# Kernel optimization log

Measured on AMD Instinct MI355X. Metric: run time of the kernel, lower is better.

## Reference

```python
import jax, jax.numpy as jnp
import numpy as np

INDIM = 256
NUM_CENTERS = 1024
OUTDIM = 128
N = 65536


def setup_inputs() -> dict:
    key = jax.random.key(0)
    kx, kc, kw, kb = jax.random.split(key, 4)
    x = jax.random.normal(kx, (N, INDIM), dtype=jnp.float32)
    # centers ~ U(-1, 1), sigmas = 0.1 as in init_centers_sigmas
    centers = jax.random.uniform(kc, (NUM_CENTERS, INDIM), dtype=jnp.float32, minval=-1.0, maxval=1.0)
    sigmas = jnp.full((NUM_CENTERS,), 0.1, dtype=jnp.float32)
    # nn.Linear(num_centers, outdim): weight [outdim, num_centers], bias [outdim]
    bound = 1.0 / np.sqrt(NUM_CENTERS)
    W = jax.random.uniform(kw, (OUTDIM, NUM_CENTERS), dtype=jnp.float32, minval=-bound, maxval=bound)
    b = jax.random.uniform(kb, (OUTDIM,), dtype=jnp.float32, minval=-bound, maxval=bound)
    return {"x": x, "centers": centers, "sigmas": sigmas, "W": W, "b": b}


def reference(x, centers, sigmas, W, b):
    # phi[n, m] = exp(-sigma_m * ||x_n - c_m||^2)
    x_sq = jnp.sum(x * x, axis=1)               # [N]
    c_sq = jnp.sum(centers * centers, axis=1)   # [M]
    cross = jnp.einsum('nd,md->nm', x, centers) # [N, M]
    sqdist = x_sq[:, None] + c_sq[None, :] - 2.0 * cross
    phi = jnp.exp(-sigmas[None, :] * sqdist)    # [N, M]
    return phi @ W.T + b                        # [N, outdim]
```

## Files before the change

kernel.cpp:

```cpp
#include <hip/hip_runtime.h>

typedef __attribute__((ext_vector_type(8))) short bf16x8;
typedef __attribute__((ext_vector_type(4))) float f32x4;
typedef unsigned int u32;
typedef unsigned long long u64;

#define LOG2E 1.44269504088896f

__device__ __forceinline__ short f2bf(float f) {
    union { float f; unsigned u; } v; v.f = f;
    unsigned r = v.u + 0x7fffu + ((v.u >> 16) & 1u);
    return (short)(r >> 16);
}

__device__ __forceinline__ u32 f2e4m3(float f) {
    u32 u = __float_as_uint(f);
    u32 sgn = (u >> 24) & 0x80u;
    u32 mag = u & 0x7fffffffu;
    if (mag >= 0x43E00000u) return sgn | 0x7Eu;
    if (mag < 0x3C800000u) {
        u32 q = (u32)(__uint_as_float(mag) * 512.0f + 0.5f);
        return sgn | q;
    }
    u32 r = mag + 0x0007FFFFu + ((mag >> 20) & 1u);
    u32 e8 = ((r >> 23) - 120u) & 0xFu;
    u32 m3 = (r >> 20) & 7u;
    return sgn | (e8 << 3) | m3;
}

__device__ __forceinline__ long pack8_e4m3(float4 a, float4 b) {
    u32 lo = f2e4m3(a.x) | (f2e4m3(a.y) << 8) | (f2e4m3(a.z) << 16) | (f2e4m3(a.w) << 24);
    u32 hi = f2e4m3(b.x) | (f2e4m3(b.y) << 8) | (f2e4m3(b.z) << 16) | (f2e4m3(b.w) << 24);
    return (long)(((u64)hi << 32) | lo);
}

#if __has_builtin(__builtin_amdgcn_exp2f)
#define EXP2(x) __builtin_amdgcn_exp2f(x)
#else
#define EXP2(x) __builtin_exp2f(x)
#endif

__device__ __forceinline__ u32 pack_bf16_trunc(float lo, float hi) {
#if __has_builtin(__builtin_amdgcn_perm)
    return __builtin_amdgcn_perm(__float_as_uint(hi), __float_as_uint(lo), 0x07060302u);
#else
    return (__float_as_uint(hi) & 0xFFFF0000u) | (__float_as_uint(lo) >> 16);
#endif
}

__device__ __forceinline__ void gload16(const void* g, void* l) {
    __builtin_amdgcn_global_load_lds(
        (const __attribute__((address_space(1))) void*)g,
        (__attribute__((address_space(3))) void*)l, 16, 0, 0);
}

__global__ __launch_bounds__(256) void rbf_prep(
    const float* __restrict__ centers, const float* __restrict__ sigmas,
    const float* __restrict__ W,
    char* __restrict__ cfrag8, short* __restrict__ wfrag,
    float* __restrict__ nsp, float* __restrict__ nscsp, float* __restrict__ tsp)
{
    const int tid = threadIdx.x;
    const int bid = blockIdx.x;
    if (bid < 256) {
        const int lane = tid & 63, w = tid >> 6;
        const int m = bid * 4 + w;
        const float4 v = ((const float4*)(centers + (size_t)m * 256))[lane];
        float s = v.x*v.x + v.y*v.y + v.z*v.z + v.w*v.w;
        #pragma unroll
        for (int off = 32; off >= 1; off >>= 1) s += __shfl_xor(s, off, 64);
        if (lane == 0) {
            const float sg = sigmas[m];
            const int c = m >> 5, w5 = m & 31;
            const int g = w5 >> 3, r = w5 & 7, h = r >> 2, j = r & 3;
            const int slot = ((c * 2 + h) * 4 + g) * 4 + j;
            nsp[slot]   = -sg * LOG2E;
            nscsp[slot] = -sg * s * LOG2E;
            tsp[slot]   = 2.0f * sg * LOG2E;
        }
    } else if (bid < 384) {
        const int s = (bid - 256) * 256 + tid;
        const int c = s >> 10, h = (s >> 9) & 1, ks = (s >> 6) & 7, lane = s & 63;
        const int l15 = lane & 15;
        const int m = c * 32 + 8 * (l15 >> 2) + 4 * h + (l15 & 3);
        const int k = ks * 32 + (lane >> 4) * 8;
        const float4 a = *(const float4*)(centers + (size_t)m * 256 + k);
        const float4 b = *(const float4*)(centers + (size_t)m * 256 + k + 4);
        *(long*)(cfrag8 + (size_t)s * 8) = pack8_e4m3(a, b);
    } else {
        const int s = (bid - 384) * 256 + tid;
        const int c = s >> 9, ot = (s >> 6) & 7, lane = s & 63;
        const int o = ot * 16 + (lane & 15);
        const int k = c * 32 + (lane >> 4) * 8;
        const float4 a = *(const float4*)(W + (size_t)o * 1024 + k);
        const float4 b = *(const float4*)(W + (size_t)o * 1024 + k + 4);
        bf16x8 t;
        t[0]=f2bf(a.x); t[1]=f2bf(a.y); t[2]=f2bf(a.z); t[3]=f2bf(a.w);
        t[4]=f2bf(b.x); t[5]=f2bf(b.y); t[6]=f2bf(b.z); t[7]=f2bf(b.w);
        ((bf16x8*)wfrag)[s] = t;
    }
}

__global__ __launch_bounds__(256, 2) void rbf_main(
    const float* __restrict__ x, const float* __restrict__ bvec,
    const char* __restrict__ cfrag8, const short* __restrict__ wfrag,
    const float* __restrict__ nsp, const float* __restrict__ nscsp,
    const float* __restrict__ tsp, float* __restrict__ out)
{
    __shared__ char   Cb8[4][8192];
    __shared__ short  Wb[4][4096];
    __shared__ float4 Tls[512];

    (void)nsp;

    const int tid = threadIdx.x;
    const int lane = tid & 63;
    const int l15 = lane & 15;
    const int g4 = lane >> 4;
    const int w = tid >> 6;
    const int qb = blockIdx.x * 128 + w * 32;

#define STAGE(ci, slot) do {                                                       \
        const char* _cs = cfrag8 + (size_t)(ci) * 8192 + w * 2048 + lane * 16;     \
        gload16(_cs,        &Cb8[(slot)][w * 2048]);                               \
        gload16(_cs + 1024, &Cb8[(slot)][w * 2048 + 1024]);                        \
        const char* _ws = (const char*)wfrag + (size_t)(ci) * 8192 + w * 2048 + lane * 16; \
        gload16(_ws,        (char*)&Wb[(slot)][0] + w * 2048);                     \
        gload16(_ws + 1024, (char*)&Wb[(slot)][0] + w * 2048 + 1024);              \
    } while (0)

#define SCHAIN(sl, d00, d01, d10, d11) do {                                        \
        const char* cb = &Cb8[(sl)][0] + (size_t)lane * 8;                         \
        _Pragma("unroll")                                                          \
        for (int ks = 0; ks < 8; ++ks) {                                           \
            const long A0 = *(const long*)(cb + ks * 512);                         \
            const long A1 = *(const long*)(cb + 4096 + ks * 512);                  \
            d00 = __builtin_amdgcn_mfma_f32_16x16x32_fp8_fp8(A0, xq8[0][ks], d00, 0, 0, 0); \
            d10 = __builtin_amdgcn_mfma_f32_16x16x32_fp8_fp8(A0, xq8[1][ks], d10, 0, 0, 0); \
            d01 = __builtin_amdgcn_mfma_f32_16x16x32_fp8_fp8(A1, xq8[0][ks], d01, 0, 0, 0); \
            d11 = __builtin_amdgcn_mfma_f32_16x16x32_fp8_fp8(A1, xq8[1][ks], d11, 0, 0, 0); \
        }                                                                          \
    } while (0)

#define FINISH(cm) do {                                                            \
        const int base0 = ((cm) * 2 + 0) * 4 + g4;                                 \
        const int base1 = ((cm) * 2 + 1) * 4 + g4;                                 \
        const float4 q0 = Tls[base0];                                              \
        const float4 t0 = Tls[256 + base0];                                        \
        const float4 q1 = Tls[base1];                                              \
        const float4 t1 = Tls[256 + base1];                                        \
        const float* q0p = (const float*)&q0; const float* t0p = (const float*)&t0;\
        const float* q1p = (const float*)&q1; const float* t1p = (const float*)&t1;\
        float p00[4], p01[4], p10[4], p11[4];                                      \
        _Pragma("unroll")                                                          \
        for (int j = 0; j < 4; ++j) {                                              \
            p00[j] = EXP2(fmaf(t0p[j], Sp00[j] - hxs0, q0p[j]));                   \
            p01[j] = EXP2(fmaf(t1p[j], Sp01[j] - hxs0, q1p[j]));                   \
            p10[j] = EXP2(fmaf(t0p[j], Sp10[j] - hxs1, q0p[j]));                   \
            p11[j] = EXP2(fmaf(t1p[j], Sp11[j] - hxs1, q1p[j]));                   \
        }                                                                          \
        union { u32 u[4]; bf16x8 v; } pa0, pa1;                                    \
        pa0.u[0] = pack_bf16_trunc(p00[0], p00[1]);                                \
        pa0.u[1] = pack_bf16_trunc(p00[2], p00[3]);                                \
        pa0.u[2] = pack_bf16_trunc(p01[0], p01[1]);                                \
        pa0.u[3] = pack_bf16_trunc(p01[2], p01[3]);                                \
        pa1.u[0] = pack_bf16_trunc(p10[0], p10[1]);                                \
        pa1.u[1] = pack_bf16_trunc(p10[2], p10[3]);                                \
        pa1.u[2] = pack_bf16_trunc(p11[0], p11[1]);                                \
        pa1.u[3] = pack_bf16_trunc(p11[2], p11[3]);                                \
        _Pragma("unroll")                                                          \
        for (int ot = 0; ot < 8; ++ot) {                                           \
            acc[0][ot] = __builtin_amdgcn_mfma_f32_16x16x32_bf16(pa0.v, wfp[ot], acc[0][ot], 0, 0, 0); \
            acc[1][ot] = __builtin_amdgcn_mfma_f32_16x16x32_bf16(pa1.v, wfp[ot], acc[1][ot], 0, 0, 0); \
        }                                                                          \
    } while (0)

    STAGE(0, 0);
    STAGE(1, 1);
    STAGE(2, 2);

    Tls[tid]       = ((const float4*)nscsp)[tid];
    Tls[256 + tid] = ((const float4*)tsp)[tid];

    long xq8[2][8];
    float xs[2];
    #pragma unroll
    for (int t = 0; t < 2; ++t) {
        const float* xr = x + (size_t)(qb + t * 16 + l15) * 256 + g4 * 8;
        float ss = 0.f;
        #pragma unroll
        for (int ks = 0; ks < 8; ++ks) {
            const float4 a = *(const float4*)(xr + ks * 32);
            const float4 b = *(const float4*)(xr + ks * 32 + 4);
            ss += a.x*a.x + a.y*a.y + a.z*a.z + a.w*a.w
                + b.x*b.x + b.y*b.y + b.z*b.z + b.w*b.w;
            xq8[t][ks] = pack8_e4m3(a, b);
        }
        ss += __shfl_xor(ss, 16, 64);
        ss += __shfl_xor(ss, 32, 64);
        xs[t] = ss;
    }
    const float hxs0 = 0.5f * xs[0];
    const float hxs1 = 0.5f * xs[1];

    f32x4 acc[2][8];
    #pragma unroll
    for (int t = 0; t < 2; ++t)
        #pragma unroll
        for (int ot = 0; ot < 8; ++ot) acc[t][ot] = (f32x4){0.f, 0.f, 0.f, 0.f};

    __syncthreads();

    STAGE(3, 3);
    bf16x8 wfp[8];
    {
        const bf16x8* wbl = (const bf16x8*)&Wb[0][0] + lane;
        #pragma unroll
        for (int f = 0; f < 8; ++f) wfp[f] = wbl[f * 64];
    }
    f32x4 Sp00 = (f32x4){0.f,0.f,0.f,0.f}, Sp01 = Sp00, Sp10 = Sp00, Sp11 = Sp00;
    __builtin_amdgcn_s_setprio(1);
    SCHAIN(0, Sp00, Sp01, Sp10, Sp11);
    __builtin_amdgcn_s_setprio(0);
    asm volatile("s_waitcnt vmcnt(8)" ::: "memory");
    __builtin_amdgcn_s_barrier();

    for (int c = 1; c < 32; ++c) {
        const int slot = c & 3;
        if (c < 29) STAGE(c + 3, (c + 3) & 3);

        bf16x8 wfc[8];
        {
            const bf16x8* wbl = (const bf16x8*)&Wb[slot][0] + lane;
            #pragma unroll
            for (int f = 0; f < 8; ++f) wfc[f] = wbl[f * 64];
        }

        __builtin_amdgcn_s_setprio(1);
        f32x4 s00 = (f32x4){0.f,0.f,0.f,0.f}, s01 = s00, s10 = s00, s11 = s00;
        SCHAIN(slot, s00, s01, s10, s11);
        FINISH(c - 1);
        __builtin_amdgcn_s_setprio(0);

        Sp00 = s00; Sp01 = s01; Sp10 = s10; Sp11 = s11;
        #pragma unroll
        for (int f = 0; f < 8; ++f) wfp[f] = wfc[f];

        if (c < 29)       asm volatile("s_waitcnt vmcnt(8)" ::: "memory");
        else if (c == 29) asm volatile("s_waitcnt vmcnt(4)" ::: "memory");
        else if (c == 30) asm volatile("s_waitcnt vmcnt(0)" ::: "memory");
        if (c < 31) __builtin_amdgcn_s_barrier();
    }

    FINISH(31);

    #pragma unroll
    for (int t = 0; t < 2; ++t) {
        #pragma unroll
        for (int jr = 0; jr < 4; ++jr) {
            const int q = qb + t * 16 + g4 * 4 + jr;
            #pragma unroll
            for (int ot = 0; ot < 8; ++ot)
                out[(size_t)q * 128 + ot * 16 + l15] = acc[t][ot][jr] + bvec[ot * 16 + l15];
        }
    }
#undef STAGE
#undef SCHAIN
#undef FINISH
}

extern "C" void kernel_launch(void* const* d_in, const int* in_sizes, int n_in,
                              void* d_out, int out_size, void* d_ws, size_t ws_size,
                              hipStream_t stream) {
    (void)in_sizes; (void)n_in; (void)out_size; (void)ws_size;
    const float* x       = (const float*)d_in[0];
    const float* centers = (const float*)d_in[1];
    const float* sigmas  = (const float*)d_in[2];
    const float* W       = (const float*)d_in[3];
    const float* b       = (const float*)d_in[4];
    float* out = (float*)d_out;

    char*  cfrag8 = (char*)d_ws;
    short* wfrag  = (short*)(cfrag8 + 32768 * 8);
    float* nsp    = (float*)(wfrag + 16384 * 8);
    float* nscsp  = nsp + 1024;
    float* tsp    = nscsp + 1024;

    rbf_prep<<<448, 256, 0, stream>>>(centers, sigmas, W, cfrag8, wfrag, nsp, nscsp, tsp);
    rbf_main<<<512, 256, 0, stream>>>(x, b, cfrag8, wfrag, nsp, nscsp, tsp, out);
}
```

Measured before the change: 70.36 us.

## Read W fragments directly from global, interleave center fragments, restructure chunk loop

W fragments now go straight from global/L2 into registers instead of being staged through LDS, which frees LDS and removes those async copies. Center fp8 fragments are repacked so each lane fetches both halves in a single 16-byte LDS read. The main loop now handles two chunks per iteration with two-deep staging and a __syncthreads, in place of the software-pipelined SCHAIN/FINISH with explicit vmcnt waits and priority hints. It also drops the unused nsp buffer. The trade-off is that W global-load latency now lands inside the loop and there is less overlap between the distance GEMM and the exp/PV stage.

After: 70.06 us. About the same (-0.4%).

```diff
diff --git a/kernel.cpp b/kernel.cpp
--- a/kernel.cpp
+++ b/kernel.cpp
@@ -2,6 +2,7 @@
 
 typedef __attribute__((ext_vector_type(8))) short bf16x8;
 typedef __attribute__((ext_vector_type(4))) float f32x4;
+typedef __attribute__((ext_vector_type(2))) long long2v;
 typedef unsigned int u32;
 typedef unsigned long long u64;
 
@@ -58,7 +59,7 @@
     const float* __restrict__ centers, const float* __restrict__ sigmas,
     const float* __restrict__ W,
     char* __restrict__ cfrag8, short* __restrict__ wfrag,
-    float* __restrict__ nsp, float* __restrict__ nscsp, float* __restrict__ tsp)
+    float* __restrict__ nscsp, float* __restrict__ tsp)
 {
     const int tid = threadIdx.x;
     const int bid = blockIdx.x;
@@ -74,21 +75,25 @@
             const int c = m >> 5, w5 = m & 31;
             const int g = w5 >> 3, r = w5 & 7, h = r >> 2, j = r & 3;
             const int slot = ((c * 2 + h) * 4 + g) * 4 + j;
-            nsp[slot]   = -sg * LOG2E;
             nscsp[slot] = -sg * s * LOG2E;
             tsp[slot]   = 2.0f * sg * LOG2E;
         }
-    } else if (bid < 384) {
+    } else if (bid < 320) {
         const int s = (bid - 256) * 256 + tid;
-        const int c = s >> 10, h = (s >> 9) & 1, ks = (s >> 6) & 7, lane = s & 63;
+        const int c = s >> 9, ks = (s >> 6) & 7, lane = s & 63;
         const int l15 = lane & 15;
-        const int m = c * 32 + 8 * (l15 >> 2) + 4 * h + (l15 & 3);
         const int k = ks * 32 + (lane >> 4) * 8;
-        const float4 a = *(const float4*)(centers + (size_t)m * 256 + k);
-        const float4 b = *(const float4*)(centers + (size_t)m * 256 + k + 4);
-        *(long*)(cfrag8 + (size_t)s * 8) = pack8_e4m3(a, b);
+        long2v t;
+        #pragma unroll
+        for (int h = 0; h < 2; ++h) {
+            const int m = c * 32 + 8 * (l15 >> 2) + 4 * h + (l15 & 3);
+            const float4 a = *(const float4*)(centers + (size_t)m * 256 + k);
+            const float4 b = *(const float4*)(centers + (size_t)m * 256 + k + 4);
+            t[h] = pack8_e4m3(a, b);
+        }
+        *(long2v*)(cfrag8 + (size_t)s * 16) = t;
     } else {
-        const int s = (bid - 384) * 256 + tid;
+        const int s = (bid - 320) * 256 + tid;
         const int c = s >> 9, ot = (s >> 6) & 7, lane = s & 63;
         const int o = ot * 16 + (lane & 15);
         const int k = c * 32 + (lane >> 4) * 8;
@@ -104,14 +109,11 @@
 __global__ __launch_bounds__(256, 2) void rbf_main(
     const float* __restrict__ x, const float* __restrict__ bvec,
     const char* __restrict__ cfrag8, const short* __restrict__ wfrag,
-    const float* __restrict__ nsp, const float* __restrict__ nscsp,
-    const float* __restrict__ tsp, float* __restrict__ out)
+    const float* __restrict__ nscsp, const float* __restrict__ tsp,
+    float* __restrict__ out)
 {
     __shared__ char   Cb8[4][8192];
-    __shared__ short  Wb[4][4096];
     __shared__ float4 Tls[512];
-
-    (void)nsp;
 
     const int tid = threadIdx.x;
     const int lane = tid & 63;
@@ -120,31 +122,25 @@
     const int w = tid >> 6;
     const int qb = blockIdx.x * 128 + w * 32;
 
-#define STAGE(ci, slot) do {                                                       \
+#define STAGEC(ci, slot) do {                                                      \
         const char* _cs = cfrag8 + (size_t)(ci) * 8192 + w * 2048 + lane * 16;     \
         gload16(_cs,        &Cb8[(slot)][w * 2048]);                               \
         gload16(_cs + 1024, &Cb8[(slot)][w * 2048 + 1024]);                        \
-        const char* _ws = (const char*)wfrag + (size_t)(ci) * 8192 + w * 2048 + lane * 16; \
-        gload16(_ws,        (char*)&Wb[(slot)][0] + w * 2048);                     \
-        gload16(_ws + 1024, (char*)&Wb[(slot)][0] + w * 2048 + 1024);              \
     } while (0)
 
-#define SCHAIN(sl, d00, d01, d10, d11) do {                                        \
-        const char* cb = &Cb8[(sl)][0] + (size_t)lane * 8;                         \
+#define SEXP(slot, cc, pa0, pa1) do {                                              \
+        f32x4 s00 = (f32x4){0.f,0.f,0.f,0.f}, s01 = s00, s10 = s00, s11 = s00;     \
+        const char* cb = &Cb8[(slot)][0] + (size_t)lane * 16;                      \
         _Pragma("unroll")                                                          \
         for (int ks = 0; ks < 8; ++ks) {                                           \
-            const long A0 = *(const long*)(cb + ks * 512);                         \
-            const long A1 = *(const long*)(cb + 4096 + ks * 512);                  \
-            d00 = __builtin_amdgcn_mfma_f32_16x16x32_fp8_fp8(A0, xq8[0][ks], d00, 0, 0, 0); \
-            d10 = __builtin_amdgcn_mfma_f32_16x16x32_fp8_fp8(A0, xq8[1][ks], d10, 0, 0, 0); \
-            d01 = __builtin_amdgcn_mfma_f32_16x16x32_fp8_fp8(A1, xq8[0][ks], d01, 0, 0, 0); \
-            d11 = __builtin_amdgcn_mfma_f32_16x16x32_fp8_fp8(A1, xq8[1][ks], d11, 0, 0, 0); \
+            const long2v A = *(const long2v*)(cb + ks * 1024);                     \
+            s00 = __builtin_amdgcn_mfma_f32_16x16x32_fp8_fp8(A[0], xq8[0][ks], s00, 0, 0, 0); \
+            s10 = __builtin_amdgcn_mfma_f32_16x16x32_fp8_fp8(A[0], xq8[1][ks], s10, 0, 0, 0); \
+            s01 = __builtin_amdgcn_mfma_f32_16x16x32_fp8_fp8(A[1], xq8[0][ks], s01, 0, 0, 0); \
+            s11 = __builtin_amdgcn_mfma_f32_16x16x32_fp8_fp8(A[1], xq8[1][ks], s11, 0, 0, 0); \
         }                                                                          \
-    } while (0)
-
-#define FINISH(cm) do {                                                            \
-        const int base0 = ((cm) * 2 + 0) * 4 + g4;                                 \
-        const int base1 = ((cm) * 2 + 1) * 4 + g4;                                 \
+        const int base0 = ((cc) * 2 + 0) * 4 + g4;                                 \
+        const int base1 = ((cc) * 2 + 1) * 4 + g4;                                 \
         const float4 q0 = Tls[base0];                                              \
         const float4 t0 = Tls[256 + base0];                                        \
         const float4 q1 = Tls[base1];                                              \
@@ -154,12 +150,11 @@
         float p00[4], p01[4], p10[4], p11[4];                                      \
         _Pragma("unroll")                                                          \
         for (int j = 0; j < 4; ++j) {                                              \
-            p00[j] = EXP2(fmaf(t0p[j], Sp00[j] - hxs0, q0p[j]));                   \
-            p01[j] = EXP2(fmaf(t1p[j], Sp01[j] - hxs0, q1p[j]));                   \
-            p10[j] = EXP2(fmaf(t0p[j], Sp10[j] - hxs1, q0p[j]));                   \
-            p11[j] = EXP2(fmaf(t1p[j], Sp11[j] - hxs1, q1p[j]));                   \
+            p00[j] = EXP2(fmaf(t0p[j], s00[j] - hxs0, q0p[j]));                    \
+            p01[j] = EXP2(fmaf(t1p[j], s01[j] - hxs0, q1p[j]));                    \
+            p10[j] = EXP2(fmaf(t0p[j], s10[j] - hxs1, q0p[j]));                    \
+            p11[j] = EXP2(fmaf(t1p[j], s11[j] - hxs1, q1p[j]));                    \
         }                                                                          \
-        union { u32 u[4]; bf16x8 v; } pa0, pa1;                                    \
         pa0.u[0] = pack_bf16_trunc(p00[0], p00[1]);                                \
         pa0.u[1] = pack_bf16_trunc(p00[2], p00[3]);                                \
         pa0.u[2] = pack_bf16_trunc(p01[0], p01[1]);                                \
@@ -168,16 +163,18 @@
         pa1.u[1] = pack_bf16_trunc(p10[2], p10[3]);                                \
         pa1.u[2] = pack_bf16_trunc(p11[0], p11[1]);                                \
         pa1.u[3] = pack_bf16_trunc(p11[2], p11[3]);                                \
+    } while (0)
+
+#define PV(pa0, pa1, wv) do {                                                      \
         _Pragma("unroll")                                                          \
         for (int ot = 0; ot < 8; ++ot) {                                           \
-            acc[0][ot] = __builtin_amdgcn_mfma_f32_16x16x32_bf16(pa0.v, wfp[ot], acc[0][ot], 0, 0, 0); \
-            acc[1][ot] = __builtin_amdgcn_mfma_f32_16x16x32_bf16(pa1.v, wfp[ot], acc[1][ot], 0, 0, 0); \
+            acc[0][ot] = __builtin_amdgcn_mfma_f32_16x16x32_bf16(pa0.v, wv[ot], acc[0][ot], 0, 0, 0); \
+            acc[1][ot] = __builtin_amdgcn_mfma_f32_16x16x32_bf16(pa1.v, wv[ot], acc[1][ot], 0, 0, 0); \
         }                                                                          \
     } while (0)
 
-    STAGE(0, 0);
-    STAGE(1, 1);
-    STAGE(2, 2);
+    STAGEC(0, 0);
+    STAGEC(1, 1);
 
     Tls[tid]       = ((const float4*)nscsp)[tid];
     Tls[256 + tid] = ((const float4*)tsp)[tid];
@@ -211,48 +208,34 @@
 
     __syncthreads();
 
-    STAGE(3, 3);
-    bf16x8 wfp[8];
-    {
-        const bf16x8* wbl = (const bf16x8*)&Wb[0][0] + lane;
-        #pragma unroll
-        for (int f = 0; f < 8; ++f) wfp[f] = wbl[f * 64];
-    }
-    f32x4 Sp00 = (f32x4){0.f,0.f,0.f,0.f}, Sp01 = Sp00, Sp10 = Sp00, Sp11 = Sp00;
-    __builtin_amdgcn_s_setprio(1);
-    SCHAIN(0, Sp00, Sp01, Sp10, Sp11);
-    __builtin_amdgcn_s_setprio(0);
-    asm volatile("s_waitcnt vmcnt(8)" ::: "memory");
-    __builtin_amdgcn_s_barrier();
-
-    for (int c = 1; c < 32; ++c) {
-        const int slot = c & 3;
-        if (c < 29) STAGE(c + 3, (c + 3) & 3);
-
-        bf16x8 wfc[8];
-        {
-            const bf16x8* wbl = (const bf16x8*)&Wb[slot][0] + lane;
-            #pragma unroll
-            for (int f = 0; f < 8; ++f) wfc[f] = wbl[f * 64];
-        }
-
-        __builtin_amdgcn_s_setprio(1);
-        f32x4 s00 = (f32x4){0.f,0.f,0.f,0.f}, s01 = s00, s10 = s00, s11 = s00;
-        SCHAIN(slot, s00, s01, s10, s11);
-        FINISH(c - 1);
-        __builtin_amdgcn_s_setprio(0);
-
-        Sp00 = s00; Sp01 = s01; Sp10 = s10; Sp11 = s11;
-        #pragma unroll
-        for (int f = 0; f < 8; ++f) wfp[f] = wfc[f];
-
-        if (c < 29)       asm volatile("s_waitcnt vmcnt(8)" ::: "memory");
-        else if (c == 29) asm volatile("s_waitcnt vmcnt(4)" ::: "memory");
-        else if (c == 30) asm volatile("s_waitcnt vmcnt(0)" ::: "memory");
-        if (c < 31) __builtin_amdgcn_s_barrier();
-    }
-
-    FINISH(31);
+    const bf16x8* wsrc = (const bf16x8*)wfrag + lane;
+
+    for (int i = 0; i < 16; ++i) {
+        const int cA = 2 * i, cB = 2 * i + 1;
+        const int sA = (i & 1) * 2, sB = sA + 1;
+
+        bf16x8 wA[8];
+        #pragma unroll
+        for (int f = 0; f < 8; ++f) wA[f] = wsrc[(size_t)cA * 512 + f * 64];
+
+        if (i < 15) {
+            STAGEC(cA + 2, sA ^ 2);
+            STAGEC(cB + 2, sB ^ 2);
+        }
+
+        union { u32 u[4]; bf16x8 v; } paA0, paA1, paB0, paB1;
+        SEXP(sA, cA, paA0, paA1);
+
+        bf16x8 wB[8];
+        #pragma unroll
+        for (int f = 0; f < 8; ++f) wB[f] = wsrc[(size_t)cB * 512 + f * 64];
+
+        PV(paA0, paA1, wA);
+        SEXP(sB, cB, paB0, paB1);
+        PV(paB0, paB1, wB);
+
+        if (i < 15) __syncthreads();
+    }
 
     #pragma unroll
     for (int t = 0; t < 2; ++t) {
@@ -264,9 +247,9 @@
                 out[(size_t)q * 128 + ot * 16 + l15] = acc[t][ot][jr] + bvec[ot * 16 + l15];
         }
     }
-#undef STAGE
-#undef SCHAIN
-#undef FINISH
+#undef STAGEC
+#undef SEXP
+#undef PV
 }
 
 extern "C" void kernel_launch(void* const* d_in, const int* in_sizes, int n_in,
@@ -281,11 +264,10 @@
     float* out = (float*)d_out;
 
     char*  cfrag8 = (char*)d_ws;
-    short* wfrag  = (short*)(cfrag8 + 32768 * 8);
-    float* nsp    = (float*)(wfrag + 16384 * 8);
-    float* nscsp  = nsp + 1024;
+    short* wfrag  = (short*)(cfrag8 + 16384 * 16);
+    float* nscsp  = (float*)(wfrag + 16384 * 8);
     float* tsp    = nscsp + 1024;
 
-    rbf_prep<<<448, 256, 0, stream>>>(centers, sigmas, W, cfrag8, wfrag, nsp, nscsp, tsp);
-    rbf_main<<<512, 256, 0, stream>>>(x, b, cfrag8, wfrag, nsp, nscsp, tsp, out);
-}
+    rbf_prep<<<384, 256, 0, stream>>>(centers, sigmas, W, cfrag8, wfrag, nscsp, tsp);
+    rbf_main<<<512, 256, 0, stream>>>(x, b, cfrag8, wfrag, nscsp, tsp, out);
+}
```
